# Performance work log

Measured on AMD Instinct MI355X. Metric: run time of the kernel, lower is better.

Reference implementation:

```python
import jax, jax.numpy as jnp
import numpy as np

B, L, D_MODEL, H, HD, FD = 1, 1024, 1024, 16, 64, 64
EPS = 1e-12

def setup_inputs() -> dict:
    key = jax.random.key(0)
    ks = jax.random.split(key, 7)
    s = 1.0 / np.sqrt(D_MODEL)
    return {
        'x': jax.random.normal(ks[0], (B, L, D_MODEL), jnp.float32),
        'Wq': jax.random.normal(ks[1], (D_MODEL, H * HD), jnp.float32) * s,
        'Wk': jax.random.normal(ks[2], (D_MODEL, H * HD), jnp.float32) * s,
        'Wv': jax.random.normal(ks[3], (D_MODEL, H * HD), jnp.float32) * s,
        'Wo': jax.random.normal(ks[4], (H * HD, D_MODEL), jnp.float32) * s,
        'Kq': jax.random.normal(ks[5], (H, HD, FD), jnp.float32) * (1.0 / np.sqrt(HD)),
        'Kk': jax.random.normal(ks[6], (H, HD, FD), jnp.float32) * (1.0 / np.sqrt(HD)),
    }

def _heads(t):
    # (b, l, h*d) -> (b, h, l, d)
    b, l, _ = t.shape
    return t.reshape(b, l, H, HD).transpose(0, 2, 1, 3)

def _feature_map(t, K):
    # UntiedHeadEinsumMLP (no skip) + SoftmaxDim with temp=1.0
    f = jnp.einsum('hdf,bhld->bhlf', K, t)
    feats = jnp.concatenate([jax.nn.softmax(f, axis=-1), jax.nn.softmax(-f, axis=-1)], axis=-1)
    return jnp.maximum(feats, EPS)  # clamp(min=eps)

def reference(x, Wq, Wk, Wv, Wo, Kq, Kk):
    q = _heads(x @ Wq)  # b h l d
    k = _heads(x @ Wk)
    v = _heads(x @ Wv)
    qf = _feature_map(q, Kq)  # b h l 2f
    kf = _feature_map(k, Kk)  # b h l 2f
    # causal linear attention: o_t = phi(q_t) . sum_{s<=t} phi(k_s) v_s^T, normalized
    kv = jnp.cumsum(kf[:, :, :, None, :] * v[..., None], axis=2)  # b h l d 2f
    o = jnp.einsum('bhlf,bhldf->bhld', qf, kv)
    z = jnp.einsum('bhlf,bhlf->bhl', qf, jnp.cumsum(kf, axis=2)) + EPS
    o = o / z[..., None]
    y = o.transpose(0, 2, 1, 3).reshape(x.shape[0], x.shape[1], H * HD)
    return y @ Wo
```

## Files before the change

kernel.cpp:

```cpp
#include <hip/hip_runtime.h>
#include <hip/hip_bf16.h>


#define NH 16
#define NC 16

using short8 = __attribute__((ext_vector_type(8))) short;
using f32x4  = __attribute__((ext_vector_type(4))) float;
typedef const __attribute__((address_space(1))) char* gptr1;
typedef __attribute__((address_space(3))) char* lptr3;

static __device__ __forceinline__ unsigned short bf16bits(float x) {
    __hip_bfloat16 h = __float2bfloat16(x);
    return __builtin_bit_cast(unsigned short, h);
}
static __device__ __forceinline__ float b2f(unsigned short u) {
    return __builtin_bit_cast(float, (unsigned int)u << 16);
}
#define SWZ(row, cb) ((cb) ^ (((row) & 7) << 4))

template<int RS>
static __device__ __forceinline__ short8 ldfrag(const char* buf, int row, int kelem) {
    return *(const short8*)(buf + row * RS + SWZ(row, kelem * 2));
}

__global__ __launch_bounds__(256) void prep(const float* __restrict__ x,
                                            const float* __restrict__ w0,
                                            const float* __restrict__ w1,
                                            const float* __restrict__ w2,
                                            const float* __restrict__ w3,
                                            const float* __restrict__ Kq,
                                            const float* __restrict__ Kk,
                                            __hip_bfloat16* __restrict__ xb,
                                            __hip_bfloat16* __restrict__ d0,
                                            __hip_bfloat16* __restrict__ d1,
                                            __hip_bfloat16* __restrict__ d2,
                                            __hip_bfloat16* __restrict__ d3,
                                            __hip_bfloat16* __restrict__ KqT,
                                            __hip_bfloat16* __restrict__ KkT) {
    const int z = blockIdx.z;
    const int tid = threadIdx.x;
    if (z < 4) {
        const float* src = (z == 0) ? w0 : (z == 1) ? w1 : (z == 2) ? w2 : w3;
        __hip_bfloat16* dst = (z == 0) ? d0 : (z == 1) ? d1 : (z == 2) ? d2 : d3;
        __shared__ float tile[64][68];
        const int bx = blockIdx.x * 64, by = blockIdx.y * 64;
#pragma unroll
        for (int j = 0; j < 4; j++) {
            const int idx = j * 256 + tid;
            const int kr = idx >> 4, c4 = idx & 15;
            float4 v = *(const float4*)&src[(size_t)(by + kr) * 1024 + bx + c4 * 4];
            *(float4*)&tile[kr][c4 * 4] = v;
        }
        __syncthreads();
        const int n = tid >> 2, k0 = (tid & 3) * 16;
        unsigned short* drow = (unsigned short*)dst + (size_t)(bx + n) * 1024 + by + k0;
#pragma unroll
        for (int q = 0; q < 4; q++) {
            ushort4 o;
            o.x = bf16bits(tile[k0 + q * 4 + 0][n]);
            o.y = bf16bits(tile[k0 + q * 4 + 1][n]);
            o.z = bf16bits(tile[k0 + q * 4 + 2][n]);
            o.w = bf16bits(tile[k0 + q * 4 + 3][n]);
            *(ushort4*)(drow + q * 4) = o;
        }
    } else if (z == 4) {
        const int blk = blockIdx.y * 16 + blockIdx.x;
#pragma unroll
        for (int j = 0; j < 4; j++) {
            const int i = blk * 4096 + j * 1024 + tid * 4;
            float4 v = *(const float4*)(x + i);
            ushort4 o;
            o.x = bf16bits(v.x); o.y = bf16bits(v.y); o.z = bf16bits(v.z); o.w = bf16bits(v.w);
            *(ushort4*)((unsigned short*)xb + i) = o;
        }
    } else {
        const int flat = blockIdx.y * 16 + blockIdx.x;
        if (flat >= 32) return;
        const int h = flat & 15;
        const float* S = (flat >> 4) ? Kk : Kq;
        __hip_bfloat16* D = (flat >> 4) ? KkT : KqT;
        __shared__ float t[64][65];
#pragma unroll
        for (int j = 0; j < 16; j++) {
            int e = tid + j * 256, r = e >> 6, c = e & 63;
            t[r][c] = S[h * 4096 + r * 64 + c];
        }
        __syncthreads();
#pragma unroll
        for (int j = 0; j < 16; j++) {
            int e = tid + j * 256, r = e >> 6, c = e & 63;
            D[h * 4096 + r * 64 + c] = __float2bfloat16(t[c][r]);
        }
    }
}

__global__ __launch_bounds__(256) void qkv_feat(const __hip_bfloat16* __restrict__ A,
                                                const __hip_bfloat16* __restrict__ B0,
                                                const __hip_bfloat16* __restrict__ B1,
                                                const __hip_bfloat16* __restrict__ B2,
                                                const __hip_bfloat16* __restrict__ KqT,
                                                const __hip_bfloat16* __restrict__ KkT,
                                                __hip_bfloat16* __restrict__ qf,
                                                __hip_bfloat16* __restrict__ kf,
                                                __hip_bfloat16* __restrict__ kfT,
                                                __hip_bfloat16* __restrict__ VT) {
    __shared__ __align__(16) char smem[49152];
    const int tid = threadIdx.x;
    const int bm = blockIdx.y * 128;
    const int which = blockIdx.x >> 4;
    const int h = blockIdx.x & 15;
    const __hip_bfloat16* B = (which == 0) ? B0 : (which == 1) ? B1 : B2;
    const int bn = h * 64;
    const int wid = tid >> 6, lane = tid & 63;
    const int g = lane >> 4, r16 = lane & 15;
    const char* Ab = (const char*)A;
    const char* Bb = (const char*)B;
    f32x4 acc[2][4] = {};

#define QKV_STAGE(dstA, dstB, kbyte)                                                                   \
    do {                                                                                               \
        _Pragma("unroll") for (int it = 0; it < 4; it++) {                                             \
            const int off = it * 4096 + tid * 16;                                                      \
            const int row = off >> 7, cb = off & 127;                                                  \
            __builtin_amdgcn_global_load_lds((gptr1)(Ab + (size_t)(bm + row) * 2048 + (kbyte) + SWZ(row, cb)), \
                                             (lptr3)((dstA) + it * 4096 + wid * 1024), 16, 0, 0);      \
        }                                                                                              \
        _Pragma("unroll") for (int it = 0; it < 2; it++) {                                             \
            const int off = it * 4096 + tid * 16;                                                      \
            const int row = off >> 7, cb = off & 127;                                                  \
            __builtin_amdgcn_global_load_lds((gptr1)(Bb + (size_t)(bn + row) * 2048 + (kbyte) + SWZ(row, cb)), \
                                             (lptr3)((dstB) + it * 4096 + wid * 1024), 16, 0, 0);      \
        }                                                                                              \
    } while (0)

    QKV_STAGE(smem, smem + 32768, 0);
    for (int kt = 0; kt < 16; kt++) {
        char* Ac = smem + ((kt & 1) ? 16384 : 0);
        char* Bc = smem + 32768 + ((kt & 1) ? 8192 : 0);
        if (kt < 15) {
            char* An = smem + ((kt & 1) ? 0 : 16384);
            char* Bn = smem + 32768 + ((kt & 1) ? 0 : 8192);
            QKV_STAGE(An, Bn, (kt + 1) * 128);
            asm volatile("s_waitcnt vmcnt(6)" ::: "memory");
        } else {
            asm volatile("s_waitcnt vmcnt(0)" ::: "memory");
        }
        __builtin_amdgcn_s_barrier();
#pragma unroll
        for (int ks = 0; ks < 2; ks++) {
            short8 af[2], bfr[4];
#pragma unroll
            for (int m = 0; m < 2; m++)
                af[m] = ldfrag<128>(Ac, wid * 32 + m * 16 + r16, ks * 32 + g * 8);
#pragma unroll
            for (int n = 0; n < 4; n++)
                bfr[n] = ldfrag<128>(Bc, n * 16 + r16, ks * 32 + g * 8);
#pragma unroll
            for (int m = 0; m < 2; m++)
#pragma unroll
                for (int n = 0; n < 4; n++)
                    acc[m][n] = __builtin_amdgcn_mfma_f32_16x16x32_bf16(af[m], bfr[n], acc[m][n], 0, 0, 0);
        }
        asm volatile("s_waitcnt lgkmcnt(0)" ::: "memory");
        __builtin_amdgcn_s_barrier();
    }
#undef QKV_STAGE

    if (which == 2) {
#pragma unroll
        for (int m = 0; m < 2; m++)
#pragma unroll
            for (int n = 0; n < 4; n++) {
                const int col = bn + n * 16 + r16;
                const int row0 = bm + wid * 32 + m * 16 + g * 4;
                ushort4 v;
                v.x = bf16bits(acc[m][n][0]); v.y = bf16bits(acc[m][n][1]);
                v.z = bf16bits(acc[m][n][2]); v.w = bf16bits(acc[m][n][3]);
                *(ushort4*)((unsigned short*)VT + (size_t)col * 1024 + row0) = v;
            }
        return;
    }

    const bool kside = (which == 1);
    char* XS = smem + 32768;
#pragma unroll
    for (int m = 0; m < 2; m++)
#pragma unroll
        for (int n = 0; n < 4; n++)
#pragma unroll
            for (int i = 0; i < 4; i++) {
                const int row = wid * 32 + m * 16 + g * 4 + i;
                *(unsigned short*)(XS + row * 128 + SWZ(row, (n * 16 + r16) * 2)) = bf16bits(acc[m][n][i]);
            }
    {
        const char* KTp = (const char*)(kside ? KkT : KqT);
#pragma unroll
        for (int it = 0; it < 2; it++) {
            const int off = it * 4096 + tid * 16;
            const int row = off >> 7, cb = off & 127;
            __builtin_amdgcn_global_load_lds((gptr1)(KTp + (size_t)(h * 64 + row) * 128 + SWZ(row, cb)),
                                             (lptr3)(smem + it * 4096 + wid * 1024), 16, 0, 0);
        }
    }
    __syncthreads();

    f32x4 fr[2][4] = {};
#pragma unroll
    for (int ks = 0; ks < 2; ks++) {
        short8 af[2], bfr[4];
#pragma unroll
        for (int m = 0; m < 2; m++)
            af[m] = ldfrag<128>(XS, wid * 32 + m * 16 + r16, ks * 32 + g * 8);
#pragma unroll
        for (int n = 0; n < 4; n++)
            bfr[n] = ldfrag<128>(smem, n * 16 + r16, ks * 32 + g * 8);
#pragma unroll
        for (int m = 0; m < 2; m++)
#pragma unroll
            for (int n = 0; n < 4; n++)
                fr[m][n] = __builtin_amdgcn_mfma_f32_16x16x32_bf16(af[m], bfr[n], fr[m][n], 0, 0, 0);
    }
    if (kside) __syncthreads();

    char* ft = smem;
    __hip_bfloat16* feat = kside ? kf : qf;
#pragma unroll
    for (int m = 0; m < 2; m++)
#pragma unroll
        for (int i = 0; i < 4; i++) {
            const int row = wid * 32 + m * 16 + g * 4 + i;
            float m1 = fr[m][0][i], m2 = -fr[m][0][i];
#pragma unroll
            for (int n = 1; n < 4; n++) {
                m1 = fmaxf(m1, fr[m][n][i]);
                m2 = fmaxf(m2, -fr[m][n][i]);
            }
#pragma unroll
            for (int off = 8; off; off >>= 1) {
                m1 = fmaxf(m1, __shfl_xor(m1, off));
                m2 = fmaxf(m2, __shfl_xor(m2, off));
            }
            float e1[4], e2[4], s1 = 0.f, s2 = 0.f;
#pragma unroll
            for (int n = 0; n < 4; n++) {
                e1[n] = __expf(fr[m][n][i] - m1);  s1 += e1[n];
                e2[n] = __expf(-fr[m][n][i] - m2); s2 += e2[n];
            }
#pragma unroll
            for (int off = 8; off; off >>= 1) {
                s1 += __shfl_xor(s1, off);
                s2 += __shfl_xor(s2, off);
            }
            const float i1 = 1.f / s1, i2 = 1.f / s2;
            __hip_bfloat16* fo = feat + ((size_t)(h * 1024 + bm + row)) * 128;
#pragma unroll
            for (int n = 0; n < 4; n++) {
                const int col = n * 16 + r16;
                unsigned short v1 = bf16bits(fmaxf(e1[n] * i1, 1e-12f));
                unsigned short v2 = bf16bits(fmaxf(e2[n] * i2, 1e-12f));
                *(unsigned short*)(fo + col) = v1;
                *(unsigned short*)(fo + col + 64) = v2;
                if (kside) {
                    *(unsigned short*)(ft + col * 256 + SWZ(col, row * 2)) = v1;
                    *(unsigned short*)(ft + (col + 64) * 256 + SWZ(col + 64, row * 2)) = v2;
                }
            }
        }
    if (kside) {
        __syncthreads();
#pragma unroll
        for (int j = 0; j < 8; j++) {
            const int off = (tid + j * 256) * 16;
            const int row = off >> 8, cb = off & 255;
            short8 v = *(const short8*)(ft + row * 256 + SWZ(row, cb));
            *(short8*)((char*)kfT + ((size_t)(h * 128 + row) * 1024 + bm) * 2 + cb) = v;
        }
    }
}

__global__ __launch_bounds__(256) void chunk_sums_mfma(const __hip_bfloat16* __restrict__ kfT,
                                                       const __hip_bfloat16* __restrict__ VT,
                                                       __hip_bfloat16* __restrict__ Scb,
                                                       float* __restrict__ ksum) {
    const int h = blockIdx.y, c = blockIdx.x, l0 = c * 64;
    __shared__ __align__(16) char VTs[64 * 128];
    __shared__ __align__(16) char KTs[128 * 128];
    const int tid = threadIdx.x, lane = tid & 63, wid = tid >> 6;
    const int r16 = lane & 15, g = lane >> 4;
#pragma unroll
    for (int it = 0; it < 2; it++) {
        const int off = it * 4096 + tid * 16;
        const int row = off >> 7, cb = off & 127;
        __builtin_amdgcn_global_load_lds((gptr1)((const char*)VT + ((size_t)(h * 64 + row) * 1024 + l0) * 2 + SWZ(row, cb)),
                                         (lptr3)(VTs + it * 4096 + wid * 1024), 16, 0, 0);
    }
#pragma unroll
    for (int it = 0; it < 4; it++) {
        const int off = it * 4096 + tid * 16;
        const int row = off >> 7, cb = off & 127;
        __builtin_amdgcn_global_load_lds((gptr1)((const char*)kfT + ((size_t)(h * 128 + row) * 1024 + l0) * 2 + SWZ(row, cb)),
                                         (lptr3)(KTs + it * 4096 + wid * 1024), 16, 0, 0);
    }
    __syncthreads();
    f32x4 acc[8] = {};
#pragma unroll
    for (int ks = 0; ks < 2; ks++) {
        short8 a = ldfrag<128>(VTs, wid * 16 + r16, ks * 32 + g * 8);
#pragma unroll
        for (int n = 0; n < 8; n++) {
            short8 b = ldfrag<128>(KTs, n * 16 + r16, ks * 32 + g * 8);
            acc[n] = __builtin_amdgcn_mfma_f32_16x16x32_bf16(a, b, acc[n], 0, 0, 0);
        }
    }
    unsigned short* o = (unsigned short*)Scb + (size_t)(h * NC + c) * 8192;
#pragma unroll
    for (int n = 0; n < 8; n++)
#pragma unroll
        for (int i = 0; i < 4; i++)
            o[(wid * 16 + g * 4 + i) * 128 + n * 16 + r16] = bf16bits(acc[n][i]);
    if (tid < 128) {
        float s = 0.f;
#pragma unroll 8
        for (int t = 0; t < 64; t++)
            s += b2f(*(const unsigned short*)(KTs + tid * 128 + SWZ(tid, t * 2)));
        ksum[(size_t)(h * NC + c) * 128 + tid] = s;
    }
}

__global__ __launch_bounds__(256) void prefix_scan(const __hip_bfloat16* __restrict__ Scb,
                                                   __hip_bfloat16* __restrict__ Sp,
                                                   const float* __restrict__ ksum,
                                                   float* __restrict__ kp) {
    const int h = blockIdx.x, eb = blockIdx.y, tid = threadIdx.x;
#pragma unroll
    for (int j = 0; j < 4; j++) {
        const int e = eb * 1024 + tid + j * 256;
        float v[NC];
#pragma unroll
        for (int c = 0; c < NC; c++)
            v[c] = b2f(((const unsigned short*)Scb)[(size_t)(h * NC + c) * 8192 + e]);
        float run = 0.f;
#pragma unroll
        for (int c = 0; c < NC; c++) {
            Sp[(size_t)(h * NC + c) * 8192 + e] = __float2bfloat16(run);
            run += v[c];
        }
    }
    if (eb == 0 && tid < 128) {
        float run = 0.f;
#pragma unroll
        for (int c = 0; c < NC; c++) {
            const size_t idx = (size_t)(h * NC + c) * 128 + tid;
            kp[idx] = run;
            run += ksum[idx];
        }
    }
}

__global__ __launch_bounds__(256) void chunk_out_mfma(const __hip_bfloat16* __restrict__ qf,
                                                      const __hip_bfloat16* __restrict__ kf,
                                                      const __hip_bfloat16* __restrict__ VT,
                                                      const __hip_bfloat16* __restrict__ Sp,
                                                      const float* __restrict__ kp,
                                                      __hip_bfloat16* __restrict__ Y) {
    const int h = blockIdx.y, c = blockIdx.x, l0 = c * 64;
    __shared__ __align__(16) char QF[64 * 256];
    __shared__ __align__(16) char KF[64 * 256];
    __shared__ __align__(16) char SP[64 * 256];
    __shared__ __align__(16) char VTs[64 * 128];
    __shared__ __align__(16) char AM[64 * 128];
    __shared__ float zi[64];
    __shared__ float invz[64];
    const int tid = threadIdx.x, lane = tid & 63, wid = tid >> 6;
    const int r16 = lane & 15, g = lane >> 4;

#pragma unroll
    for (int it = 0; it < 4; it++) {
        const int off = it * 4096 + wid * 1024 + lane * 16;
        const int row = off >> 8, cb = off & 255;
        const int sw = SWZ(row, cb);
        __builtin_amdgcn_global_load_lds((gptr1)((const char*)qf + ((size_t)(h * 1024 + l0 + row)) * 256 + sw),
                                         (lptr3)(QF + it * 4096 + wid * 1024), 16, 0, 0);
        __builtin_amdgcn_global_load_lds((gptr1)((const char*)kf + ((size_t)(h * 1024 + l0 + row)) * 256 + sw),
                                         (lptr3)(KF + it * 4096 + wid * 1024), 16, 0, 0);
        __builtin_amdgcn_global_load_lds((gptr1)((const char*)Sp + ((size_t)((h * NC + c) * 64 + row)) * 256 + sw),
                                         (lptr3)(SP + it * 4096 + wid * 1024), 16, 0, 0);
    }
#pragma unroll
    for (int it = 0; it < 2; it++) {
        const int off = it * 4096 + wid * 1024 + lane * 16;
        const int row = off >> 7, cb = off & 127;
        __builtin_amdgcn_global_load_lds((gptr1)((const char*)VT + ((size_t)(h * 64 + row) * 1024 + l0) * 2 + SWZ(row, cb)),
                                         (lptr3)(VTs + it * 4096 + wid * 1024), 16, 0, 0);
    }
    __syncthreads();

    f32x4 a4[4] = {};
#pragma unroll
    for (int ks = 0; ks < 4; ks++) {
        short8 a = ldfrag<256>(QF, wid * 16 + r16, ks * 32 + g * 8);
#pragma unroll
        for (int n = 0; n < 4; n++) {
            short8 bb = ldfrag<256>(KF, n * 16 + r16, ks * 32 + g * 8);
            a4[n] = __builtin_amdgcn_mfma_f32_16x16x32_bf16(a, bb, a4[n], 0, 0, 0);
        }
    }
    const int rowl = wid * 16 + g * 4;
#pragma unroll
    for (int i = 0; i < 4; i++) {
        float r = 0.f;
#pragma unroll
        for (int n = 0; n < 4; n++) {
            const int col = n * 16 + r16;
            float v = (col <= rowl + i) ? a4[n][i] : 0.f;
            a4[n][i] = v;
            r += v;
        }
#pragma unroll
        for (int off = 8; off; off >>= 1) r += __shfl_xor(r, off);
        if (r16 == 0) zi[rowl + i] = r;
#pragma unroll
        for (int n = 0; n < 4; n++)
            *(unsigned short*)(AM + (rowl + i) * 128 + SWZ(rowl + i, (n * 16 + r16) * 2)) = bf16bits(a4[n][i]);
    }
    __syncthreads();

    if (tid < 64) {
        float z = zi[tid] + 1e-12f;
        const float* kpp = kp + (size_t)(h * NC + c) * 128;
#pragma unroll 8
        for (int f = 0; f < 128; f++)
            z += b2f(*(const unsigned short*)(QF + tid * 256 + SWZ(tid, f * 2))) * kpp[f];
        invz[tid] = 1.f / z;
    }

    f32x4 o4[4] = {};
#pragma unroll
    for (int ks = 0; ks < 2; ks++) {
        short8 a = ldfrag<128>(AM, wid * 16 + r16, ks * 32 + g * 8);
#pragma unroll
        for (int n = 0; n < 4; n++) {
            short8 bb = ldfrag<128>(VTs, n * 16 + r16, ks * 32 + g * 8);
            o4[n] = __builtin_amdgcn_mfma_f32_16x16x32_bf16(a, bb, o4[n], 0, 0, 0);
        }
    }
#pragma unroll
    for (int ks = 0; ks < 4; ks++) {
        short8 a = ldfrag<256>(QF, wid * 16 + r16, ks * 32 + g * 8);
#pragma unroll
        for (int n = 0; n < 4; n++) {
            short8 bb = ldfrag<256>(SP, n * 16 + r16, ks * 32 + g * 8);
            o4[n] = __builtin_amdgcn_mfma_f32_16x16x32_bf16(a, bb, o4[n], 0, 0, 0);
        }
    }
    __syncthreads();
#pragma unroll
    for (int n = 0; n < 4; n++)
#pragma unroll
        for (int i = 0; i < 4; i++) {
            const int row = rowl + i, col = n * 16 + r16;
            Y[((size_t)(l0 + row)) * 1024 + h * 64 + col] = __float2bfloat16(o4[n][i] * invz[row]);
        }
}

__global__ __launch_bounds__(256) void gemm_final(const __hip_bfloat16* __restrict__ A,
                                                  const __hip_bfloat16* __restrict__ B,
                                                  float* __restrict__ C) {
    __shared__ __align__(16) char smem[32768];
    const int tid = threadIdx.x;
    const int bm = blockIdx.y * 64, bn = blockIdx.x * 64;
    const int wid = tid >> 6, lane = tid & 63;
    const int g = lane >> 4, r16 = lane & 15;
    const int wr = wid >> 1, wc = wid & 1;
    const char* Ab = (const char*)A;
    const char* Bb = (const char*)B;
    f32x4 acc[2][2] = {};

#define FIN_STAGE(dstA, dstB, kbyte)                                                                   \
    do {                                                                                               \
        _Pragma("unroll") for (int it = 0; it < 2; it++) {                                             \
            const int off = it * 4096 + tid * 16;                                                      \
            const int row = off >> 7, cb = off & 127;                                                  \
            __builtin_amdgcn_global_load_lds((gptr1)(Ab + (size_t)(bm + row) * 2048 + (kbyte) + SWZ(row, cb)), \
                                             (lptr3)((dstA) + it * 4096 + wid * 1024), 16, 0, 0);      \
            __builtin_amdgcn_global_load_lds((gptr1)(Bb + (size_t)(bn + row) * 2048 + (kbyte) + SWZ(row, cb)), \
                                             (lptr3)((dstB) + it * 4096 + wid * 1024), 16, 0, 0);      \
        }                                                                                              \
    } while (0)

    FIN_STAGE(smem, smem + 16384, 0);
    for (int kt = 0; kt < 16; kt++) {
        char* Ac = smem + ((kt & 1) ? 8192 : 0);
        char* Bc = smem + 16384 + ((kt & 1) ? 8192 : 0);
        if (kt < 15) {
            char* An = smem + ((kt & 1) ? 0 : 8192);
            char* Bn = smem + 16384 + ((kt & 1) ? 0 : 8192);
            FIN_STAGE(An, Bn, (kt + 1) * 128);
            asm volatile("s_waitcnt vmcnt(4)" ::: "memory");
        } else {
            asm volatile("s_waitcnt vmcnt(0)" ::: "memory");
        }
        __builtin_amdgcn_s_barrier();
#pragma unroll
        for (int ks = 0; ks < 2; ks++) {
            short8 af[2], bfr[2];
#pragma unroll
            for (int m = 0; m < 2; m++)
                af[m] = ldfrag<128>(Ac, wr * 32 + m * 16 + r16, ks * 32 + g * 8);
#pragma unroll
            for (int n = 0; n < 2; n++)
                bfr[n] = ldfrag<128>(Bc, wc * 32 + n * 16 + r16, ks * 32 + g * 8);
#pragma unroll
            for (int m = 0; m < 2; m++)
#pragma unroll
                for (int n = 0; n < 2; n++)
                    acc[m][n] = __builtin_amdgcn_mfma_f32_16x16x32_bf16(af[m], bfr[n], acc[m][n], 0, 0, 0);
        }
        asm volatile("s_waitcnt lgkmcnt(0)" ::: "memory");
        __builtin_amdgcn_s_barrier();
    }
#undef FIN_STAGE
#pragma unroll
    for (int m = 0; m < 2; m++)
#pragma unroll
        for (int n = 0; n < 2; n++)
#pragma unroll
            for (int i = 0; i < 4; i++) {
                const int row = bm + wr * 32 + m * 16 + g * 4 + i;
                const int col = bn + wc * 32 + n * 16 + r16;
                C[(size_t)row * 1024 + col] = acc[m][n][i];
            }
}

extern "C" void kernel_launch(void* const* d_in, const int* in_sizes, int n_in,
                              void* d_out, int out_size, void* d_ws, size_t ws_size,
                              hipStream_t stream) {
    const float* x  = (const float*)d_in[0];
    const float* Wq = (const float*)d_in[1];
    const float* Wk = (const float*)d_in[2];
    const float* Wv = (const float*)d_in[3];
    const float* Wo = (const float*)d_in[4];
    const float* Kq = (const float*)d_in[5];
    const float* Kk = (const float*)d_in[6];
    float* out = (float*)d_out;
    float* ws = (float*)d_ws;

    const size_t M1 = 1024 * 1024;
    if (ws_size < 10 * M1 * sizeof(float)) return;

    __hip_bfloat16* xb  = (__hip_bfloat16*)(ws);
    __hip_bfloat16* Wqt = (__hip_bfloat16*)(ws + M1 / 2);
    __hip_bfloat16* Wkt = (__hip_bfloat16*)(ws + 1 * M1);
    __hip_bfloat16* Wvt = (__hip_bfloat16*)(ws + 3 * M1 / 2);
    __hip_bfloat16* Wot = (__hip_bfloat16*)(ws + 2 * M1);
    __hip_bfloat16* KqT = (__hip_bfloat16*)(ws + 5 * M1 / 2);
    __hip_bfloat16* KkT = (__hip_bfloat16*)(ws + 5 * M1 / 2 + 32768);
    __hip_bfloat16* VT  = (__hip_bfloat16*)(ws + 3 * M1);
    __hip_bfloat16* qfb = (__hip_bfloat16*)(ws + 7 * M1 / 2);
    __hip_bfloat16* kfb = (__hip_bfloat16*)(ws + 9 * M1 / 2);
    __hip_bfloat16* kfT = (__hip_bfloat16*)(ws + 11 * M1 / 2);
    __hip_bfloat16* Scb = (__hip_bfloat16*)(ws + 13 * M1 / 2);
    __hip_bfloat16* Spb = (__hip_bfloat16*)(ws + 15 * M1 / 2);
    __hip_bfloat16* Yb  = (__hip_bfloat16*)(ws + 17 * M1 / 2);
    float* ksum = ws + 9 * M1;
    float* kp   = ws + 9 * M1 + 32768;

    prep<<<dim3(16, 16, 6), 256, 0, stream>>>(x, Wq, Wk, Wv, Wo, Kq, Kk,
                                              xb, Wqt, Wkt, Wvt, Wot, KqT, KkT);
    qkv_feat<<<dim3(48, 8), 256, 0, stream>>>(xb, Wqt, Wkt, Wvt, KqT, KkT, qfb, kfb, kfT, VT);
    chunk_sums_mfma<<<dim3(NC, NH), 256, 0, stream>>>(kfT, VT, Scb, ksum);
    prefix_scan<<<dim3(NH, 8), 256, 0, stream>>>(Scb, Spb, ksum, kp);
    chunk_out_mfma<<<dim3(NC, NH), 256, 0, stream>>>(qfb, kfb, VT, Spb, kp, Yb);
    gemm_final<<<dim3(16, 16), 256, 0, stream>>>(Yb, Wot, out);
}
```

Measured before the change: 54.83 us.

## Enlarge tiles in QKV-feature and final GEMM kernels to cut block count

The QKV projection kernel now computes a 128x128 output tile covering two heads per block, so it launches 24x8 blocks instead of 48x8. The feature-map MLP and softmax now loop over both heads, and the LDS layout is reworked to 64 KB to hold both. The final output GEMM goes from 64x64 to 128x64 tiles, halving its grid to 16x8. This raises reuse of the A tiles and per-warp MFMA density, at the cost of fewer blocks on a 256-CU device and higher register and LDS pressure.

```diff
diff --git a/kernel.cpp b/kernel.cpp
--- a/kernel.cpp
+++ b/kernel.cpp
@@ -95,83 +95,80 @@
     }
 }
 
-__global__ __launch_bounds__(256) void qkv_feat(const __hip_bfloat16* __restrict__ A,
-                                                const __hip_bfloat16* __restrict__ B0,
-                                                const __hip_bfloat16* __restrict__ B1,
-                                                const __hip_bfloat16* __restrict__ B2,
-                                                const __hip_bfloat16* __restrict__ KqT,
-                                                const __hip_bfloat16* __restrict__ KkT,
-                                                __hip_bfloat16* __restrict__ qf,
-                                                __hip_bfloat16* __restrict__ kf,
-                                                __hip_bfloat16* __restrict__ kfT,
-                                                __hip_bfloat16* __restrict__ VT) {
-    __shared__ __align__(16) char smem[49152];
+__global__ __launch_bounds__(256) void qkv_feat2(const __hip_bfloat16* __restrict__ A,
+                                                 const __hip_bfloat16* __restrict__ B0,
+                                                 const __hip_bfloat16* __restrict__ B1,
+                                                 const __hip_bfloat16* __restrict__ B2,
+                                                 const __hip_bfloat16* __restrict__ KqT,
+                                                 const __hip_bfloat16* __restrict__ KkT,
+                                                 __hip_bfloat16* __restrict__ qf,
+                                                 __hip_bfloat16* __restrict__ kf,
+                                                 __hip_bfloat16* __restrict__ kfT,
+                                                 __hip_bfloat16* __restrict__ VT) {
+    __shared__ __align__(16) char smem[65536];
     const int tid = threadIdx.x;
     const int bm = blockIdx.y * 128;
-    const int which = blockIdx.x >> 4;
-    const int h = blockIdx.x & 15;
+    const int which = blockIdx.x >> 3;
+    const int nb2 = blockIdx.x & 7;
     const __hip_bfloat16* B = (which == 0) ? B0 : (which == 1) ? B1 : B2;
-    const int bn = h * 64;
+    const int bn = nb2 * 128;
+    const int h0 = nb2 * 2;
     const int wid = tid >> 6, lane = tid & 63;
     const int g = lane >> 4, r16 = lane & 15;
     const char* Ab = (const char*)A;
     const char* Bb = (const char*)B;
-    f32x4 acc[2][4] = {};
-
-#define QKV_STAGE(dstA, dstB, kbyte)                                                                   \
+    f32x4 acc[2][8] = {};
+
+#define QKV_STAGE2(dstA, dstB, kbyte)                                                                  \
     do {                                                                                               \
         _Pragma("unroll") for (int it = 0; it < 4; it++) {                                             \
             const int off = it * 4096 + tid * 16;                                                      \
             const int row = off >> 7, cb = off & 127;                                                  \
             __builtin_amdgcn_global_load_lds((gptr1)(Ab + (size_t)(bm + row) * 2048 + (kbyte) + SWZ(row, cb)), \
                                              (lptr3)((dstA) + it * 4096 + wid * 1024), 16, 0, 0);      \
-        }                                                                                              \
-        _Pragma("unroll") for (int it = 0; it < 2; it++) {                                             \
-            const int off = it * 4096 + tid * 16;                                                      \
-            const int row = off >> 7, cb = off & 127;                                                  \
             __builtin_amdgcn_global_load_lds((gptr1)(Bb + (size_t)(bn + row) * 2048 + (kbyte) + SWZ(row, cb)), \
                                              (lptr3)((dstB) + it * 4096 + wid * 1024), 16, 0, 0);      \
         }                                                                                              \
     } while (0)
 
-    QKV_STAGE(smem, smem + 32768, 0);
+    QKV_STAGE2(smem, smem + 32768, 0);
     for (int kt = 0; kt < 16; kt++) {
         char* Ac = smem + ((kt & 1) ? 16384 : 0);
-        char* Bc = smem + 32768 + ((kt & 1) ? 8192 : 0);
+        char* Bc = smem + 32768 + ((kt & 1) ? 16384 : 0);
         if (kt < 15) {
             char* An = smem + ((kt & 1) ? 0 : 16384);
-            char* Bn = smem + 32768 + ((kt & 1) ? 0 : 8192);
-            QKV_STAGE(An, Bn, (kt + 1) * 128);
-            asm volatile("s_waitcnt vmcnt(6)" ::: "memory");
+            char* Bn = smem + 32768 + ((kt & 1) ? 0 : 16384);
+            QKV_STAGE2(An, Bn, (kt + 1) * 128);
+            asm volatile("s_waitcnt vmcnt(8)" ::: "memory");
         } else {
             asm volatile("s_waitcnt vmcnt(0)" ::: "memory");
         }
         __builtin_amdgcn_s_barrier();
 #pragma unroll
         for (int ks = 0; ks < 2; ks++) {
-            short8 af[2], bfr[4];
+            short8 af[2], bfr[8];
 #pragma unroll
             for (int m = 0; m < 2; m++)
                 af[m] = ldfrag<128>(Ac, wid * 32 + m * 16 + r16, ks * 32 + g * 8);
 #pragma unroll
-            for (int n = 0; n < 4; n++)
+            for (int n = 0; n < 8; n++)
                 bfr[n] = ldfrag<128>(Bc, n * 16 + r16, ks * 32 + g * 8);
 #pragma unroll
             for (int m = 0; m < 2; m++)
 #pragma unroll
-                for (int n = 0; n < 4; n++)
+                for (int n = 0; n < 8; n++)
                     acc[m][n] = __builtin_amdgcn_mfma_f32_16x16x32_bf16(af[m], bfr[n], acc[m][n], 0, 0, 0);
         }
         asm volatile("s_waitcnt lgkmcnt(0)" ::: "memory");
         __builtin_amdgcn_s_barrier();
     }
-#undef QKV_STAGE
+#undef QKV_STAGE2
 
     if (which == 2) {
 #pragma unroll
         for (int m = 0; m < 2; m++)
 #pragma unroll
-            for (int n = 0; n < 4; n++) {
+            for (int n = 0; n < 8; n++) {
                 const int col = bn + n * 16 + r16;
                 const int row0 = bm + wid * 32 + m * 16 + g * 4;
                 ushort4 v;
@@ -183,98 +180,107 @@
     }
 
     const bool kside = (which == 1);
-    char* XS = smem + 32768;
+    char* XS = smem;
 #pragma unroll
     for (int m = 0; m < 2; m++)
 #pragma unroll
-        for (int n = 0; n < 4; n++)
+        for (int n = 0; n < 8; n++)
 #pragma unroll
             for (int i = 0; i < 4; i++) {
                 const int row = wid * 32 + m * 16 + g * 4 + i;
-                *(unsigned short*)(XS + row * 128 + SWZ(row, (n * 16 + r16) * 2)) = bf16bits(acc[m][n][i]);
+                const int hh = n >> 2;
+                const int d = (n & 3) * 16 + r16;
+                *(unsigned short*)(XS + hh * 16384 + row * 128 + SWZ(row, d * 2)) = bf16bits(acc[m][n][i]);
             }
     {
         const char* KTp = (const char*)(kside ? KkT : KqT);
 #pragma unroll
-        for (int it = 0; it < 2; it++) {
-            const int off = it * 4096 + tid * 16;
-            const int row = off >> 7, cb = off & 127;
-            __builtin_amdgcn_global_load_lds((gptr1)(KTp + (size_t)(h * 64 + row) * 128 + SWZ(row, cb)),
-                                             (lptr3)(smem + it * 4096 + wid * 1024), 16, 0, 0);
-        }
+        for (int hh = 0; hh < 2; hh++)
+#pragma unroll
+            for (int it = 0; it < 2; it++) {
+                const int off = it * 4096 + tid * 16;
+                const int row = off >> 7, cb = off & 127;
+                __builtin_amdgcn_global_load_lds((gptr1)(KTp + (size_t)((h0 + hh) * 64 + row) * 128 + SWZ(row, cb)),
+                                                 (lptr3)(smem + 32768 + hh * 8192 + it * 4096 + wid * 1024), 16, 0, 0);
+            }
     }
     __syncthreads();
 
-    f32x4 fr[2][4] = {};
-#pragma unroll
-    for (int ks = 0; ks < 2; ks++) {
-        short8 af[2], bfr[4];
+    f32x4 fr[2][2][4] = {};
+#pragma unroll
+    for (int ks = 0; ks < 2; ks++)
+#pragma unroll
+        for (int hh = 0; hh < 2; hh++) {
+            short8 a_[2];
+#pragma unroll
+            for (int m = 0; m < 2; m++)
+                a_[m] = ldfrag<128>(XS + hh * 16384, wid * 32 + m * 16 + r16, ks * 32 + g * 8);
+#pragma unroll
+            for (int n = 0; n < 4; n++) {
+                short8 b = ldfrag<128>(smem + 32768 + hh * 8192, n * 16 + r16, ks * 32 + g * 8);
+#pragma unroll
+                for (int m = 0; m < 2; m++)
+                    fr[hh][m][n] = __builtin_amdgcn_mfma_f32_16x16x32_bf16(a_[m], b, fr[hh][m][n], 0, 0, 0);
+            }
+        }
+    __syncthreads();
+
+    char* ft = smem + 32768;
+    __hip_bfloat16* feat = kside ? kf : qf;
+#pragma unroll
+    for (int hh = 0; hh < 2; hh++) {
 #pragma unroll
         for (int m = 0; m < 2; m++)
-            af[m] = ldfrag<128>(XS, wid * 32 + m * 16 + r16, ks * 32 + g * 8);
-#pragma unroll
-        for (int n = 0; n < 4; n++)
-            bfr[n] = ldfrag<128>(smem, n * 16 + r16, ks * 32 + g * 8);
-#pragma unroll
-        for (int m = 0; m < 2; m++)
-#pragma unroll
-            for (int n = 0; n < 4; n++)
-                fr[m][n] = __builtin_amdgcn_mfma_f32_16x16x32_bf16(af[m], bfr[n], fr[m][n], 0, 0, 0);
-    }
-    if (kside) __syncthreads();
-
-    char* ft = smem;
-    __hip_bfloat16* feat = kside ? kf : qf;
-#pragma unroll
-    for (int m = 0; m < 2; m++)
-#pragma unroll
-        for (int i = 0; i < 4; i++) {
-            const int row = wid * 32 + m * 16 + g * 4 + i;
-            float m1 = fr[m][0][i], m2 = -fr[m][0][i];
-#pragma unroll
-            for (int n = 1; n < 4; n++) {
-                m1 = fmaxf(m1, fr[m][n][i]);
-                m2 = fmaxf(m2, -fr[m][n][i]);
-            }
-#pragma unroll
-            for (int off = 8; off; off >>= 1) {
-                m1 = fmaxf(m1, __shfl_xor(m1, off));
-                m2 = fmaxf(m2, __shfl_xor(m2, off));
-            }
-            float e1[4], e2[4], s1 = 0.f, s2 = 0.f;
-#pragma unroll
-            for (int n = 0; n < 4; n++) {
-                e1[n] = __expf(fr[m][n][i] - m1);  s1 += e1[n];
-                e2[n] = __expf(-fr[m][n][i] - m2); s2 += e2[n];
-            }
-#pragma unroll
-            for (int off = 8; off; off >>= 1) {
-                s1 += __shfl_xor(s1, off);
-                s2 += __shfl_xor(s2, off);
-            }
-            const float i1 = 1.f / s1, i2 = 1.f / s2;
-            __hip_bfloat16* fo = feat + ((size_t)(h * 1024 + bm + row)) * 128;
-#pragma unroll
-            for (int n = 0; n < 4; n++) {
-                const int col = n * 16 + r16;
-                unsigned short v1 = bf16bits(fmaxf(e1[n] * i1, 1e-12f));
-                unsigned short v2 = bf16bits(fmaxf(e2[n] * i2, 1e-12f));
-                *(unsigned short*)(fo + col) = v1;
-                *(unsigned short*)(fo + col + 64) = v2;
-                if (kside) {
-                    *(unsigned short*)(ft + col * 256 + SWZ(col, row * 2)) = v1;
-                    *(unsigned short*)(ft + (col + 64) * 256 + SWZ(col + 64, row * 2)) = v2;
+#pragma unroll
+            for (int i = 0; i < 4; i++) {
+                const int row = wid * 32 + m * 16 + g * 4 + i;
+                float m1 = fr[hh][m][0][i], m2 = -fr[hh][m][0][i];
+#pragma unroll
+                for (int n = 1; n < 4; n++) {
+                    m1 = fmaxf(m1, fr[hh][m][n][i]);
+                    m2 = fmaxf(m2, -fr[hh][m][n][i]);
                 }
-            }
-        }
-    if (kside) {
-        __syncthreads();
-#pragma unroll
-        for (int j = 0; j < 8; j++) {
-            const int off = (tid + j * 256) * 16;
-            const int row = off >> 8, cb = off & 255;
-            short8 v = *(const short8*)(ft + row * 256 + SWZ(row, cb));
-            *(short8*)((char*)kfT + ((size_t)(h * 128 + row) * 1024 + bm) * 2 + cb) = v;
+#pragma unroll
+                for (int off = 8; off; off >>= 1) {
+                    m1 = fmaxf(m1, __shfl_xor(m1, off));
+                    m2 = fmaxf(m2, __shfl_xor(m2, off));
+                }
+                float e1[4], e2[4], s1 = 0.f, s2 = 0.f;
+#pragma unroll
+                for (int n = 0; n < 4; n++) {
+                    e1[n] = __expf(fr[hh][m][n][i] - m1);  s1 += e1[n];
+                    e2[n] = __expf(-fr[hh][m][n][i] - m2); s2 += e2[n];
+                }
+#pragma unroll
+                for (int off = 8; off; off >>= 1) {
+                    s1 += __shfl_xor(s1, off);
+                    s2 += __shfl_xor(s2, off);
+                }
+                const float i1 = 1.f / s1, i2 = 1.f / s2;
+                __hip_bfloat16* fo = feat + ((size_t)((h0 + hh) * 1024 + bm + row)) * 128;
+#pragma unroll
+                for (int n = 0; n < 4; n++) {
+                    const int col = n * 16 + r16;
+                    unsigned short v1 = bf16bits(fmaxf(e1[n] * i1, 1e-12f));
+                    unsigned short v2 = bf16bits(fmaxf(e2[n] * i2, 1e-12f));
+                    *(unsigned short*)(fo + col) = v1;
+                    *(unsigned short*)(fo + col + 64) = v2;
+                    if (kside) {
+                        *(unsigned short*)(ft + col * 256 + SWZ(col, row * 2)) = v1;
+                        *(unsigned short*)(ft + (col + 64) * 256 + SWZ(col + 64, row * 2)) = v2;
+                    }
+                }
+            }
+        if (kside) {
+            __syncthreads();
+#pragma unroll
+            for (int j = 0; j < 8; j++) {
+                const int off = (tid + j * 256) * 16;
+                const int row = off >> 8, cb = off & 255;
+                short8 v = *(const short8*)(ft + row * 256 + SWZ(row, cb));
+                *(short8*)((char*)kfT + (((size_t)(h0 + hh) * 128 + row) * 1024 + bm) * 2 + cb) = v;
+            }
+            __syncthreads();
         }
     }
 }
@@ -467,54 +473,57 @@
 __global__ __launch_bounds__(256) void gemm_final(const __hip_bfloat16* __restrict__ A,
                                                   const __hip_bfloat16* __restrict__ B,
                                                   float* __restrict__ C) {
-    __shared__ __align__(16) char smem[32768];
+    __shared__ __align__(16) char smem[49152];
     const int tid = threadIdx.x;
-    const int bm = blockIdx.y * 64, bn = blockIdx.x * 64;
+    const int bm = blockIdx.y * 128, bn = blockIdx.x * 64;
     const int wid = tid >> 6, lane = tid & 63;
     const int g = lane >> 4, r16 = lane & 15;
-    const int wr = wid >> 1, wc = wid & 1;
     const char* Ab = (const char*)A;
     const char* Bb = (const char*)B;
-    f32x4 acc[2][2] = {};
+    f32x4 acc[2][4] = {};
 
 #define FIN_STAGE(dstA, dstB, kbyte)                                                                   \
     do {                                                                                               \
-        _Pragma("unroll") for (int it = 0; it < 2; it++) {                                             \
+        _Pragma("unroll") for (int it = 0; it < 4; it++) {                                             \
             const int off = it * 4096 + tid * 16;                                                      \
             const int row = off >> 7, cb = off & 127;                                                  \
             __builtin_amdgcn_global_load_lds((gptr1)(Ab + (size_t)(bm + row) * 2048 + (kbyte) + SWZ(row, cb)), \
                                              (lptr3)((dstA) + it * 4096 + wid * 1024), 16, 0, 0);      \
+        }                                                                                              \
+        _Pragma("unroll") for (int it = 0; it < 2; it++) {                                             \
+            const int off = it * 4096 + tid * 16;                                                      \
+            const int row = off >> 7, cb = off & 127;                                                  \
             __builtin_amdgcn_global_load_lds((gptr1)(Bb + (size_t)(bn + row) * 2048 + (kbyte) + SWZ(row, cb)), \
                                              (lptr3)((dstB) + it * 4096 + wid * 1024), 16, 0, 0);      \
         }                                                                                              \
     } while (0)
 
-    FIN_STAGE(smem, smem + 16384, 0);
+    FIN_STAGE(smem, smem + 32768, 0);
     for (int kt = 0; kt < 16; kt++) {
-        char* Ac = smem + ((kt & 1) ? 8192 : 0);
-        char* Bc = smem + 16384 + ((kt & 1) ? 8192 : 0);
+        char* Ac = smem + ((kt & 1) ? 16384 : 0);
+        char* Bc = smem + 32768 + ((kt & 1) ? 8192 : 0);
         if (kt < 15) {
-            char* An = smem + ((kt & 1) ? 0 : 8192);
-            char* Bn = smem + 16384 + ((kt & 1) ? 0 : 8192);
+            char* An = smem + ((kt & 1) ? 0 : 16384);
+            char* Bn = smem + 32768 + ((kt & 1) ? 0 : 8192);
             FIN_STAGE(An, Bn, (kt + 1) * 128);
-            asm volatile("s_waitcnt vmcnt(4)" ::: "memory");
+            asm volatile("s_waitcnt vmcnt(6)" ::: "memory");
         } else {
             asm volatile("s_waitcnt vmcnt(0)" ::: "memory");
         }
         __builtin_amdgcn_s_barrier();
 #pragma unroll
         for (int ks = 0; ks < 2; ks++) {
-            short8 af[2], bfr[2];
+            short8 af[2], bfr[4];
 #pragma unroll
             for (int m = 0; m < 2; m++)
-                af[m] = ldfrag<128>(Ac, wr * 32 + m * 16 + r16, ks * 32 + g * 8);
-#pragma unroll
-            for (int n = 0; n < 2; n++)
-                bfr[n] = ldfrag<128>(Bc, wc * 32 + n * 16 + r16, ks * 32 + g * 8);
+                af[m] = ldfrag<128>(Ac, wid * 32 + m * 16 + r16, ks * 32 + g * 8);
+#pragma unroll
+            for (int n = 0; n < 4; n++)
+                bfr[n] = ldfrag<128>(Bc, n * 16 + r16, ks * 32 + g * 8);
 #pragma unroll
             for (int m = 0; m < 2; m++)
 #pragma unroll
-                for (int n = 0; n < 2; n++)
+                for (int n = 0; n < 4; n++)
                     acc[m][n] = __builtin_amdgcn_mfma_f32_16x16x32_bf16(af[m], bfr[n], acc[m][n], 0, 0, 0);
         }
         asm volatile("s_waitcnt lgkmcnt(0)" ::: "memory");
@@ -524,11 +533,11 @@
 #pragma unroll
     for (int m = 0; m < 2; m++)
 #pragma unroll
-        for (int n = 0; n < 2; n++)
+        for (int n = 0; n < 4; n++)
 #pragma unroll
             for (int i = 0; i < 4; i++) {
-                const int row = bm + wr * 32 + m * 16 + g * 4 + i;
-                const int col = bn + wc * 32 + n * 16 + r16;
+                const int row = bm + wid * 32 + m * 16 + g * 4 + i;
+                const int col = bn + n * 16 + r16;
                 C[(size_t)row * 1024 + col] = acc[m][n][i];
             }
 }
@@ -568,9 +577,9 @@
 
     prep<<<dim3(16, 16, 6), 256, 0, stream>>>(x, Wq, Wk, Wv, Wo, Kq, Kk,
                                               xb, Wqt, Wkt, Wvt, Wot, KqT, KkT);
-    qkv_feat<<<dim3(48, 8), 256, 0, stream>>>(xb, Wqt, Wkt, Wvt, KqT, KkT, qfb, kfb, kfT, VT);
+    qkv_feat2<<<dim3(24, 8), 256, 0, stream>>>(xb, Wqt, Wkt, Wvt, KqT, KkT, qfb, kfb, kfT, VT);
     chunk_sums_mfma<<<dim3(NC, NH), 256, 0, stream>>>(kfT, VT, Scb, ksum);
     prefix_scan<<<dim3(NH, 8), 256, 0, stream>>>(Scb, Spb, ksum, kp);
     chunk_out_mfma<<<dim3(NC, NH), 256, 0, stream>>>(qfb, kfb, VT, Spb, kp, Yb);
-    gemm_final<<<dim3(16, 16), 256, 0, stream>>>(Yb, Wot, out);
-}
+    gemm_final<<<dim3(16, 8), 256, 0, stream>>>(Yb, Wot, out);
+}
```

Measured after the change: 63.12 us. 1.15x slower.
